# Kernel optimization log

Hardware: AMD Instinct MI355X
Metric: run time of the kernel (lower is better)

Reference implementation:

```python
import jax, jax.numpy as jnp
import numpy as np

B, N, A = 8, 16384, 7
NUM_GROUP = 1024   # npoint / G
GROUP_SIZE = 32    # knn k / M


def setup_inputs() -> dict:
    key = jax.random.key(0)
    xyz = jax.random.uniform(key, (B, N, A), dtype=jnp.float32)
    return {"xyz": xyz}


def _farthest_point_sample(xyz, npoint):
    # xyz: [B, N, A]; distances computed on first 3 dims only.
    b, n, a = xyz.shape
    coords = xyz[:, :, :3]
    batch = jnp.arange(b)
    # Deterministic start index (original uses randint; any start is a valid FPS seed).
    init = (jnp.full((b, n), 1e10, dtype=xyz.dtype), jnp.zeros((b,), dtype=jnp.int32))

    def step(carry, _):
        distance, farthest = carry
        centroid = xyz[batch, farthest]                      # [B, A]
        d = jnp.sum((coords - centroid[:, None, :3]) ** 2, -1)  # [B, N]
        distance = jnp.minimum(distance, d)                  # masked update == min
        new_farthest = jnp.argmax(distance, axis=-1).astype(jnp.int32)
        return (distance, new_farthest), (farthest, centroid)

    _, (idxs, cents) = jax.lax.scan(step, init, None, length=npoint)
    centroids = jnp.swapaxes(idxs, 0, 1)        # [B, npoint]
    centroids_attrs = jnp.swapaxes(cents, 0, 1)  # [B, npoint, A]
    return centroids, centroids_attrs


def _knn(center, xyz, k):
    # Euclidean cdist over ALL A attributes (as in the original torch.cdist call).
    # Squared distance preserves topk ordering.
    c2 = jnp.sum(center ** 2, -1)[:, :, None]    # [B, G, 1]
    x2 = jnp.sum(xyz ** 2, -1)[:, None, :]       # [B, 1, N]
    d2 = c2 + x2 - 2.0 * jnp.einsum('bga,bna->bgn', center, xyz)  # [B, G, N]
    _, idx = jax.lax.top_k(-d2, k)               # smallest-k, ascending distance
    return idx


def reference(xyz):
    center_idx, centroids_attrs = _farthest_point_sample(xyz, NUM_GROUP)
    centroids_coors = centroids_attrs[:, :, :3]
    idx = _knn(centroids_attrs, xyz, GROUP_SIZE)             # [B, G, M]
    b = xyz.shape[0]
    neighborhood = xyz[jnp.arange(b)[:, None, None], idx]    # [B, G, M, A]
    neighborhood = jnp.concatenate(
        [neighborhood[..., :3] - centroids_coors[:, :, None, :],
         neighborhood[..., 3:]], axis=-1)
    return neighborhood, center_idx, centroids_attrs, centroids_coors
```

## Files before the change

kernel.cpp:

```cpp
#include <hip/hip_runtime.h>

#define N_PTS  16384
#define B_SZ   8
#define NGROUP 1024
#define KNN_K  32
#define ATTR   7

#define OFF_NB     0
#define OFF_IDX    (B_SZ * NGROUP * KNN_K * ATTR)
#define OFF_CATTR  (OFF_IDX + B_SZ * NGROUP)
#define OFF_CCOORD (OFF_CATTR + B_SZ * NGROUP * ATTR)

typedef float v2f __attribute__((ext_vector_type(2)));
typedef float f2u __attribute__((ext_vector_type(2), aligned(4)));

template <int CTRL>
__device__ __forceinline__ float fmax_dpp_step(float x) {
    int d = __builtin_amdgcn_update_dpp(__float_as_int(x), __float_as_int(x),
                                        CTRL, 0xf, 0xf, false);
    return fmaxf(x, __int_as_float(d));
}
template <int CTRL>
__device__ __forceinline__ unsigned umin_dpp_step(unsigned x) {
    unsigned d = (unsigned)__builtin_amdgcn_update_dpp((int)x, (int)x,
                                                       CTRL, 0xf, 0xf, false);
    return x < d ? x : d;
}

__device__ __forceinline__ float wave_max_f32(float x) {
    x = fmax_dpp_step<0x111>(x);
    x = fmax_dpp_step<0x112>(x);
    x = fmax_dpp_step<0x114>(x);
    x = fmax_dpp_step<0x118>(x);
    x = fmax_dpp_step<0x142>(x);
    x = fmax_dpp_step<0x143>(x);
    return __int_as_float(__builtin_amdgcn_readlane(__float_as_int(x), 63));
}
__device__ __forceinline__ unsigned wave_min_u32(unsigned x) {
    x = umin_dpp_step<0x111>(x);
    x = umin_dpp_step<0x112>(x);
    x = umin_dpp_step<0x114>(x);
    x = umin_dpp_step<0x118>(x);
    x = umin_dpp_step<0x142>(x);
    x = umin_dpp_step<0x143>(x);
    return (unsigned)__builtin_amdgcn_readlane((int)x, 63);
}

__global__ void prep_kernel(const float* __restrict__ xyz, float* __restrict__ x2,
                            float* __restrict__ xt) {
#pragma clang fp contract(off)
    int i = blockIdx.x * blockDim.x + threadIdx.x;
    if (i >= B_SZ * N_PTS) return;
    const int b = i >> 14;
    const int p = i & (N_PTS - 1);
    const float* q = xyz + (size_t)i * ATTR;
    f2u a01 = *(const f2u*)q;
    f2u a23 = *(const f2u*)(q + 2);
    f2u a45 = *(const f2u*)(q + 4);
    float a6 = q[6];
    float s = a01.x * a01.x;
    s = s + a01.y * a01.y;
    s = s + a23.x * a23.x;
    s = s + a23.y * a23.y;
    s = s + a45.x * a45.x;
    s = s + a45.y * a45.y;
    s = s + a6 * a6;
    x2[i] = s;
    float* T = xt + (size_t)b * ATTR * N_PTS + p;
    T[0 * N_PTS] = a01.x;
    T[1 * N_PTS] = a01.y;
    T[2 * N_PTS] = a23.x;
    T[3 * N_PTS] = a23.y;
    T[4 * N_PTS] = a45.x;
    T[5 * N_PTS] = a45.y;
    T[6 * N_PTS] = a6;
}

#define FOR16(M) M(0) M(1) M(2) M(3) M(4) M(5) M(6) M(7) \
                 M(8) M(9) M(10) M(11) M(12) M(13) M(14) M(15)

#define PT_DECL(J) v2f px##J, py##J, pz##J, pd##J;

#define PT_LOAD(J) { \
    const int p0 = t + ((2 * J) << 9); \
    const float* q0 = X + (size_t)p0 * ATTR; \
    const float* q1 = q0 + (size_t)512 * ATTR; \
    f2u u0 = *(const volatile f2u*)q0; float z0 = ((const volatile float*)q0)[2]; \
    f2u u1 = *(const volatile f2u*)q1; float z1 = ((const volatile float*)q1)[2]; \
    px##J = (v2f){u0.x, u1.x}; \
    py##J = (v2f){u0.y, u1.y}; \
    pz##J = (v2f){z0, z1}; \
    pd##J = (v2f){1e10f, 1e10f}; }

#define PT_STEP(J) { \
    v2f dx = px##J - cx2; \
    v2f dy = py##J - cy2; \
    v2f dz = pz##J - cz2; \
    v2f a  = dx * dx; \
    a = a + dy * dy; \
    a = a + dz * dz; \
    v2f nd; \
    nd.x = fminf(pd##J.x, a.x); \
    nd.y = fminf(pd##J.y, a.y); \
    pd##J = nd; \
    if (nd.x > best) { best = nd.x; bidx = t + ((2 * J) << 9); } \
    if (nd.y > best) { best = nd.y; bidx = t + ((2 * J + 1) << 9); } }

__global__ __launch_bounds__(512)
__attribute__((amdgpu_waves_per_eu(2, 2)))
void fps_kernel(const float* __restrict__ xyz, float* __restrict__ out) {
#pragma clang fp contract(off)
    const int b = blockIdx.x;
    const int t = threadIdx.x;
    const int lane = t & 63;
    const float* X = xyz + (size_t)b * N_PTS * ATTR;

    FOR16(PT_DECL)
    FOR16(PT_LOAD)

    __shared__ unsigned long long slot[3];
    __shared__ int sel[NGROUP];
    if (t == 0) { slot[0] = 0ull; sel[0] = 0; }
    float cx = X[0], cy = X[1], cz = X[2];
    __syncthreads();

    for (int s = 0; s < NGROUP - 1; ++s) {
        const v2f cx2 = {cx, cx}, cy2 = {cy, cy}, cz2 = {cz, cz};
        float best = -1.0f;
        int   bidx = 0;
        FOR16(PT_STEP)
        const float wm = wave_max_f32(best);
        const unsigned cand = (best == wm) ? (unsigned)bidx : 0xFFFFFFFFu;
        const unsigned widx = wave_min_u32(cand);
        if (lane == 0) {
            const unsigned long long key =
                ((unsigned long long)__float_as_uint(wm) << 32) |
                (unsigned)(N_PTS - widx);
            atomicMax(&slot[s % 3], key);
        }
        if (t == 0) slot[(s + 1) % 3] = 0ull;
        __syncthreads();
        const unsigned long long bk = slot[s % 3];
        const int win = N_PTS - (int)(unsigned)bk;
        const int sbidx = __builtin_amdgcn_readfirstlane(win);
        if (t == 0) sel[s + 1] = sbidx;
        const float* q = X + (size_t)sbidx * ATTR;
        cx = q[0]; cy = q[1]; cz = q[2];
    }
    __syncthreads();

    for (int g = t; g < NGROUP; g += 512) {
        const int idx = sel[g];
        const float* q = X + (size_t)idx * ATTR;
        float a0 = q[0], a1 = q[1], a2 = q[2], a3 = q[3], a4 = q[4], a5 = q[5], a6 = q[6];
        out[OFF_IDX + b * NGROUP + g] = (float)idx;
        float* ca = out + OFF_CATTR + (size_t)(b * NGROUP + g) * ATTR;
        ca[0] = a0; ca[1] = a1; ca[2] = a2; ca[3] = a3; ca[4] = a4; ca[5] = a5; ca[6] = a6;
        float* cc = out + OFF_CCOORD + (size_t)(b * NGROUP + g) * 3;
        cc[0] = a0; cc[1] = a1; cc[2] = a2;
    }
}

__device__ __forceinline__ void topk_insert(float d2, int p, int lane,
                                            float& ld, int& li, float& kd, int& ki) {
    const bool cand = (d2 < kd) || (d2 == kd && p < ki);
    unsigned long long mask = __ballot(cand);
    while (mask) {
        const int l = __ffsll(mask) - 1;
        mask &= mask - 1;
        const float dc = __shfl(d2, l);
        const int   pc = __shfl(p, l);
        if ((dc < kd) || (dc == kd && pc < ki)) {
            const bool before = (ld < dc) || (ld == dc && li < pc);
            const int pos = (int)__popcll(__ballot(before));
            const float sd = __shfl_up(ld, 1);
            const int   si = __shfl_up(li, 1);
            if (lane == pos)      { ld = dc; li = pc; }
            else if (lane > pos)  { ld = sd; li = si; }
            if (lane >= KNN_K)    { ld = __builtin_inff(); li = 0x7fffffff; }
            kd = __shfl(ld, KNN_K - 1);
            ki = __shfl(li, KNN_K - 1);
        }
    }
}

__global__ __launch_bounds__(256) void knn_kernel(const float* __restrict__ xyz,
                                                  const float* __restrict__ x2,
                                                  const float* __restrict__ xt,
                                                  float* __restrict__ out) {
#pragma clang fp contract(off)
    const int lane = threadIdx.x & 63;
    const int w    = threadIdx.x >> 6;
    const int gib  = w >> 1;
    const int half = w & 1;
    const int gg = blockIdx.x * 2 + gib;
    const int b  = gg >> 10;
    const float* X = xyz + (size_t)b * N_PTS * ATTR;

    const float* C = out + OFF_CATTR + (size_t)gg * ATTR;
    const float c0 = C[0], c1 = C[1], c2a = C[2], c3 = C[3], c4 = C[4], c5 = C[5], c6 = C[6];
    float csq = c0 * c0;
    csq = csq + c1 * c1;
    csq = csq + c2a * c2a;
    csq = csq + c3 * c3;
    csq = csq + c4 * c4;
    csq = csq + c5 * c5;
    csq = csq + c6 * c6;

    float ld = __builtin_inff();
    int   li = 0x7fffffff;
    float kd = __builtin_inff();
    int   ki = 0x7fffffff;

    const int pbeg = half * (N_PTS / 2);
    const int pend = pbeg + (N_PTS / 2);

    if (xt != nullptr) {
        const float* T0 = xt + (size_t)b * ATTR * N_PTS;
        const float* T1 = T0 + N_PTS;
        const float* T2 = T1 + N_PTS;
        const float* T3 = T2 + N_PTS;
        const float* T4 = T3 + N_PTS;
        const float* T5 = T4 + N_PTS;
        const float* T6 = T5 + N_PTS;
        const float* XB = x2 + (size_t)b * N_PTS;
        for (int p0 = pbeg; p0 < pend; p0 += 64) {
            const int p = p0 + lane;
            const float q0 = T0[p], q1 = T1[p], q2 = T2[p], q3 = T3[p];
            const float q4 = T4[p], q5 = T5[p], q6 = T6[p];
            float dot = c0 * q0;
            dot = dot + c1 * q1;
            dot = dot + c2a * q2;
            dot = dot + c3 * q3;
            dot = dot + c4 * q4;
            dot = dot + c5 * q5;
            dot = dot + c6 * q6;
            const float xx = XB[p];
            const float d2 = (csq + xx) - 2.0f * dot;
            topk_insert(d2, p, lane, ld, li, kd, ki);
        }
    } else {
        for (int p0 = pbeg; p0 < pend; p0 += 64) {
            const int p = p0 + lane;
            const float* q = X + (size_t)p * ATTR;
            float dot = c0 * q[0];
            dot = dot + c1 * q[1];
            dot = dot + c2a * q[2];
            dot = dot + c3 * q[3];
            dot = dot + c4 * q[4];
            dot = dot + c5 * q[5];
            dot = dot + c6 * q[6];
            float xx = q[0] * q[0];
            xx = xx + q[1] * q[1];
            xx = xx + q[2] * q[2];
            xx = xx + q[3] * q[3];
            xx = xx + q[4] * q[4];
            xx = xx + q[5] * q[5];
            xx = xx + q[6] * q[6];
            const float d2 = (csq + xx) - 2.0f * dot;
            topk_insert(d2, p, lane, ld, li, kd, ki);
        }
    }

    __shared__ float smd[2][2][KNN_K];
    __shared__ int   smi[2][2][KNN_K];
    if (lane < KNN_K) {
        smd[gib][half][lane] = ld;
        smi[gib][half][lane] = li;
    }
    __syncthreads();

    if (half == 0) {
        const float dc2 = (lane < KNN_K) ? smd[gib][1][lane] : __builtin_inff();
        const int   pc2 = (lane < KNN_K) ? smi[gib][1][lane] : 0x7fffffff;
        topk_insert(dc2, pc2, lane, ld, li, kd, ki);

        if (lane < KNN_K) {
            const float* q = X + (size_t)li * ATTR;
            float* o = out + OFF_NB + ((size_t)gg * KNN_K + lane) * ATTR;
            o[0] = q[0] - c0;
            o[1] = q[1] - c1;
            o[2] = q[2] - c2a;
            o[3] = q[3];
            o[4] = q[4];
            o[5] = q[5];
            o[6] = q[6];
        }
    }
}

extern "C" void kernel_launch(void* const* d_in, const int* in_sizes, int n_in,
                              void* d_out, int out_size, void* d_ws, size_t ws_size,
                              hipStream_t stream) {
    const float* xyz = (const float*)d_in[0];
    float* out = (float*)d_out;

    const size_t need = (size_t)(B_SZ * N_PTS) * (1 + ATTR) * sizeof(float);
    const bool use_ws = ws_size >= need;
    float* x2 = use_ws ? (float*)d_ws : nullptr;
    float* xt = use_ws ? ((float*)d_ws + B_SZ * N_PTS) : nullptr;

    if (use_ws) {
        prep_kernel<<<(B_SZ * N_PTS + 255) / 256, 256, 0, stream>>>(xyz, x2, xt);
    }
    fps_kernel<<<B_SZ, 512, 0, stream>>>(xyz, out);
    knn_kernel<<<(B_SZ * NGROUP) / 2, 256, 0, stream>>>(xyz, x2, xt, out);
}
```

Baseline: 1.948 ms.

## Share LDS-staged point chunks across four groups per block in kNN

Each wave now processes one full group over all points instead of two waves splitting a group's points. Blocks stage transposed point attributes and squared norms into shared memory in 1024-point chunks, reused by the four groups in the block. This removes the cross-wave top-k merge and cuts redundant global loads. In exchange, each wave's serial insert chain is twice as long, and per-chunk barriers couple waves with uneven insertion work.

```diff
diff --git a/kernel.cpp b/kernel.cpp
--- a/kernel.cpp
+++ b/kernel.cpp
@@ -5,6 +5,7 @@
 #define NGROUP 1024
 #define KNN_K  32
 #define ATTR   7
+#define CHUNK  1024
 
 #define OFF_NB     0
 #define OFF_IDX    (B_SZ * NGROUP * KNN_K * ATTR)
@@ -191,9 +192,7 @@
 #pragma clang fp contract(off)
     const int lane = threadIdx.x & 63;
     const int w    = threadIdx.x >> 6;
-    const int gib  = w >> 1;
-    const int half = w & 1;
-    const int gg = blockIdx.x * 2 + gib;
+    const int gg = blockIdx.x * 4 + w;
     const int b  = gg >> 10;
     const float* X = xyz + (size_t)b * N_PTS * ATTR;
 
@@ -212,35 +211,42 @@
     float kd = __builtin_inff();
     int   ki = 0x7fffffff;
 
-    const int pbeg = half * (N_PTS / 2);
-    const int pend = pbeg + (N_PTS / 2);
-
     if (xt != nullptr) {
+        __shared__ float sm[8][CHUNK];
         const float* T0 = xt + (size_t)b * ATTR * N_PTS;
-        const float* T1 = T0 + N_PTS;
-        const float* T2 = T1 + N_PTS;
-        const float* T3 = T2 + N_PTS;
-        const float* T4 = T3 + N_PTS;
-        const float* T5 = T4 + N_PTS;
-        const float* T6 = T5 + N_PTS;
         const float* XB = x2 + (size_t)b * N_PTS;
-        for (int p0 = pbeg; p0 < pend; p0 += 64) {
-            const int p = p0 + lane;
-            const float q0 = T0[p], q1 = T1[p], q2 = T2[p], q3 = T3[p];
-            const float q4 = T4[p], q5 = T5[p], q6 = T6[p];
-            float dot = c0 * q0;
-            dot = dot + c1 * q1;
-            dot = dot + c2a * q2;
-            dot = dot + c3 * q3;
-            dot = dot + c4 * q4;
-            dot = dot + c5 * q5;
-            dot = dot + c6 * q6;
-            const float xx = XB[p];
-            const float d2 = (csq + xx) - 2.0f * dot;
-            topk_insert(d2, p, lane, ld, li, kd, ki);
+        for (int cb = 0; cb < N_PTS; cb += CHUNK) {
+            __syncthreads();
+#pragma unroll
+            for (int a = 0; a < 7; ++a) {
+                const float* Ta = T0 + (size_t)a * N_PTS + cb;
+#pragma unroll
+                for (int off = 0; off < CHUNK; off += 256)
+                    sm[a][off + threadIdx.x] = Ta[off + threadIdx.x];
+            }
+#pragma unroll
+            for (int off = 0; off < CHUNK; off += 256)
+                sm[7][off + threadIdx.x] = XB[cb + off + threadIdx.x];
+            __syncthreads();
+            for (int pp = 0; pp < CHUNK; pp += 64) {
+                const int j = pp + lane;
+                const int p = cb + j;
+                const float q0 = sm[0][j], q1 = sm[1][j], q2 = sm[2][j], q3 = sm[3][j];
+                const float q4 = sm[4][j], q5 = sm[5][j], q6 = sm[6][j];
+                float dot = c0 * q0;
+                dot = dot + c1 * q1;
+                dot = dot + c2a * q2;
+                dot = dot + c3 * q3;
+                dot = dot + c4 * q4;
+                dot = dot + c5 * q5;
+                dot = dot + c6 * q6;
+                const float xx = sm[7][j];
+                const float d2 = (csq + xx) - 2.0f * dot;
+                topk_insert(d2, p, lane, ld, li, kd, ki);
+            }
         }
     } else {
-        for (int p0 = pbeg; p0 < pend; p0 += 64) {
+        for (int p0 = 0; p0 < N_PTS; p0 += 64) {
             const int p = p0 + lane;
             const float* q = X + (size_t)p * ATTR;
             float dot = c0 * q[0];
@@ -262,30 +268,16 @@
         }
     }
 
-    __shared__ float smd[2][2][KNN_K];
-    __shared__ int   smi[2][2][KNN_K];
     if (lane < KNN_K) {
-        smd[gib][half][lane] = ld;
-        smi[gib][half][lane] = li;
-    }
-    __syncthreads();
-
-    if (half == 0) {
-        const float dc2 = (lane < KNN_K) ? smd[gib][1][lane] : __builtin_inff();
-        const int   pc2 = (lane < KNN_K) ? smi[gib][1][lane] : 0x7fffffff;
-        topk_insert(dc2, pc2, lane, ld, li, kd, ki);
-
-        if (lane < KNN_K) {
-            const float* q = X + (size_t)li * ATTR;
-            float* o = out + OFF_NB + ((size_t)gg * KNN_K + lane) * ATTR;
-            o[0] = q[0] - c0;
-            o[1] = q[1] - c1;
-            o[2] = q[2] - c2a;
-            o[3] = q[3];
-            o[4] = q[4];
-            o[5] = q[5];
-            o[6] = q[6];
-        }
+        const float* q = X + (size_t)li * ATTR;
+        float* o = out + OFF_NB + ((size_t)gg * KNN_K + lane) * ATTR;
+        o[0] = q[0] - c0;
+        o[1] = q[1] - c1;
+        o[2] = q[2] - c2a;
+        o[3] = q[3];
+        o[4] = q[4];
+        o[5] = q[5];
+        o[6] = q[6];
     }
 }
 
@@ -304,5 +296,5 @@
         prep_kernel<<<(B_SZ * N_PTS + 255) / 256, 256, 0, stream>>>(xyz, x2, xt);
     }
     fps_kernel<<<B_SZ, 512, 0, stream>>>(xyz, out);
-    knn_kernel<<<(B_SZ * NGROUP) / 2, 256, 0, stream>>>(xyz, x2, xt, out);
-}
+    knn_kernel<<<(B_SZ * NGROUP) / 4, 256, 0, stream>>>(xyz, x2, xt, out);
+}
```

Result: faster. 1.905 ms (-2.2%).
